# Kernel tuning notes

Measured on AMD Instinct MI355X. Metric: run time of the kernel, lower is better.

The kernel has to match this reference:

```python
import jax, jax.numpy as jnp
import numpy as np

B, C, L = 2, 256, 2048   # batch, emb_dim, seq_len
D, H = 64, 8             # d_model (per-head), n_heads
HD = D * H
EPS = 1e-8


def glob_ln(x, gamma, beta):
    # x: (B, C, L); normalize over all non-batch dims, affine over channel dim 1
    mean = jnp.mean(x, axis=(1, 2), keepdims=True)
    var = jnp.mean((x - mean) ** 2, axis=(1, 2), keepdims=True)
    normed = (x - mean) / jnp.sqrt(var + EPS)
    return gamma[None, :, None] * normed + beta[None, :, None]


def pos_encoding(length, dim):
    pos = jnp.arange(length, dtype=jnp.float32)[:, None]
    div = jnp.exp(jnp.arange(0, dim, 2, dtype=jnp.float32) * (-np.log(10000.0) / dim))
    ang = pos * div  # (L, dim/2)
    return jnp.stack([jnp.sin(ang), jnp.cos(ang)], axis=-1).reshape(length, dim)


def setup_inputs() -> dict:
    key = jax.random.key(0)
    ks = jax.random.split(key, 16)
    s_in = 1.0 / np.sqrt(C)
    s_hd = 1.0 / np.sqrt(HD)
    return {
        "x": jax.random.normal(ks[0], (B, C, L), dtype=jnp.float32),
        "Wq": jax.random.uniform(ks[1], (HD, C), minval=-s_in, maxval=s_in),
        "bq": jax.random.uniform(ks[2], (HD,), minval=-s_in, maxval=s_in),
        "Wk": jax.random.uniform(ks[3], (HD, C), minval=-s_in, maxval=s_in),
        "bk": jax.random.uniform(ks[4], (HD,), minval=-s_in, maxval=s_in),
        "Wv": jax.random.uniform(ks[5], (HD, C), minval=-s_in, maxval=s_in),
        "bv": jax.random.uniform(ks[6], (HD,), minval=-s_in, maxval=s_in),
        "Wo": jax.random.uniform(ks[7], (C, HD), minval=-s_hd, maxval=s_hd),
        "bo": jax.random.uniform(ks[8], (C,), minval=-s_hd, maxval=s_hd),
        "g_mha": jnp.ones((C,)), "b_mha": jnp.zeros((C,)),
        "conv_w": jax.random.uniform(ks[9], (C, C), minval=-s_in, maxval=s_in),
        "conv_b": jax.random.uniform(ks[10], (C,), minval=-s_in, maxval=s_in),
        "g_ffn": jnp.ones((C,)), "b_ffn": jnp.zeros((C,)),
        "alpha": jnp.float32(0.25),
        "g_out": jnp.ones((C,)), "b_out": jnp.zeros((C,)),
    }


def reference(x, Wq, bq, Wk, bk, Wv, bv, Wo, bo, g_mha, b_mha,
              conv_w, conv_b, g_ffn, b_ffn, alpha, g_out, b_out):
    scale = 1.0 / np.sqrt(D)
    t = jnp.transpose(x, (0, 2, 1))            # (B, L, C)
    t = t + pos_encoding(L, C)[None]
    # multi-head attention (self)
    q = (scale * (t @ Wq.T + bq)).reshape(B, L, H, D)
    k = (t @ Wk.T + bk).reshape(B, L, H, D)
    v = (t @ Wv.T + bv).reshape(B, L, H, D)
    scores = jnp.einsum('nlhd,nshd->nhls', q, k)  # (B, H, L, L)
    attn = jax.nn.softmax(scores, axis=-1)
    o = jnp.einsum('nhls,nshd->nlhd', attn, v).reshape(B, L, HD)
    t = t + (o @ Wo.T + bo)                    # residual
    y = glob_ln(jnp.transpose(t, (0, 2, 1)), g_mha, b_mha)  # (B, C, L)
    # FFN: 1x1 conv + GlobLN + PReLU
    f = jnp.einsum('bcl,oc->bol', y, conv_w) + conv_b[None, :, None]
    f = glob_ln(f, g_ffn, b_ffn)
    f = jnp.where(f >= 0, f, alpha * f)
    return glob_ln(f + y, g_out, b_out)
```

## Files before the change

### kernel.cpp

```cpp
#include <hip/hip_runtime.h>
#include <hip/hip_bf16.h>
#include <math.h>

#define BB   2
#define CC   256
#define LL   2048
#define DD   64
#define HH   8
#define HDIM 512
#define BLQ  (BB*LL)
#define EPSV 1e-8f
#define QSCALE (0.125f * 1.44269504088896f)

typedef __attribute__((ext_vector_type(8))) short short8;
typedef __attribute__((ext_vector_type(4))) float f32x4;

__device__ __forceinline__ float wred_sum(float v) {
#pragma unroll
    for (int off = 32; off > 0; off >>= 1) v += __shfl_down(v, off, 64);
    return v;
}
__device__ __forceinline__ unsigned pk(float a, float b) {
    unsigned r;
    asm("v_cvt_pk_bf16_f32 %0, %1, %2" : "=v"(r) : "v"(a), "v"(b));
    return r;
}
__device__ __forceinline__ float ex2(float x) {
    float r;
    asm("v_exp_f32 %0, %1" : "=v"(r) : "v"(x));
    return r;
}
__device__ __forceinline__ float lg2(float x) {
    float r;
    asm("v_log_f32 %0, %1" : "=v"(r) : "v"(x));
    return r;
}
__device__ __forceinline__ float bf2f(unsigned short v) {
    union { unsigned u; float f; } c; c.u = ((unsigned)v) << 16; return c.f;
}
__device__ __forceinline__ short8 ld_frag(const unsigned short* p) {
    union { short8 v; uint2 u[2]; } f;
    f.u[0] = *(const uint2*)p;
    f.u[1] = *(const uint2*)(p + 4);
    return f.v;
}

__global__ __launch_bounds__(256) void k_prep(const float* __restrict__ x,
                                              const float* __restrict__ Wq, const float* __restrict__ Wk,
                                              const float* __restrict__ Wv, const float* __restrict__ Wo,
                                              const float* __restrict__ Wc,
                                              float* __restrict__ t,
                                              unsigned short* __restrict__ tb,
                                              unsigned short* __restrict__ dqkv,
                                              unsigned short* __restrict__ dWo,
                                              unsigned short* __restrict__ dWc) {
    int bid = blockIdx.x;
    int tid = threadIdx.x;
    if (bid >= 256) {
        int idx = ((bid - 256) * 256 + tid) * 4;
        const float* s; unsigned short* d;
        if (idx < 131072)      { s = Wq + idx;          d = dqkv + idx; }
        else if (idx < 262144) { s = Wk + idx - 131072; d = dqkv + idx; }
        else if (idx < 393216) { s = Wv + idx - 262144; d = dqkv + idx; }
        else if (idx < 524288) { s = Wo + idx - 393216; d = dWo + idx - 393216; }
        else                   { s = Wc + idx - 524288; d = dWc + idx - 524288; }
        float4 v = *(const float4*)s;
        uint2 u; u.x = pk(v.x, v.y); u.y = pk(v.z, v.w);
        *(uint2*)d = u;
        return;
    }
    __shared__ float tr[64][65];
    int l0 = (bid & 31) * 64, c0 = ((bid >> 5) & 3) * 64, b = bid >> 7;
    int r = tid >> 2, q = tid & 3;
#pragma unroll
    for (int p = 0; p < 4; ++p) {
        int lc = 4 * (q + 4 * p);
        float4 v = *(const float4*)&x[((size_t)(b * CC + c0 + r)) * LL + l0 + lc];
        tr[lc + 0][r] = v.x; tr[lc + 1][r] = v.y; tr[lc + 2][r] = v.z; tr[lc + 3][r] = v.w;
    }
    __syncthreads();
    int lg = l0 + r;
#pragma unroll
    for (int p = 0; p < 4; ++p) {
        int cc = 4 * (q + 4 * p);
        float4 v = *(const float4*)&tr[r][cc];
        float pe[4];
#pragma unroll
        for (int i = 0; i < 4; ++i) {
            int cg = c0 + cc + i;
            float freq = __expf((float)(cg & ~1) * (-9.210340371976184f / (float)CC));
            float ang = (float)lg * freq;
            pe[i] = (cg & 1) ? __cosf(ang) : __sinf(ang);
        }
        v.x += pe[0]; v.y += pe[1]; v.z += pe[2]; v.w += pe[3];
        size_t o = ((size_t)(b * LL + lg)) * CC + c0 + cc;
        *(float4*)&t[o] = v;
        uint2 u; u.x = pk(v.x, v.y); u.y = pk(v.z, v.w);
        *(uint2*)&tb[o] = u;
    }
}

#define MLDK 68
__global__ __launch_bounds__(256) void k_mm(const unsigned short* __restrict__ A,
                                            const unsigned short* __restrict__ W,
                                            const float* __restrict__ b0,
                                            const float* __restrict__ b1,
                                            const float* __restrict__ b2,
                                            const float* resid,
                                            float* out, unsigned short* outb,
                                            float* pstat,
                                            int mode, int M, int N, int K) {
    __shared__ unsigned short As[2][64][MLDK];
    __shared__ unsigned short Ws[2][64][MLDK];
    __shared__ float rs[4][2];
    int tid = threadIdx.x;
    int w = tid >> 6, lane = tid & 63, g = lane >> 4, qi = lane & 15;
    int bm = blockIdx.x * 64, bn = blockIdx.y * 64;
    int wr = w >> 1, wc = w & 1;
    int srow = tid >> 2, sq = tid & 3;
    bool vseg = (mode == 1) && (bn >= 1024);
    f32x4 acc[2][2];
    acc[0][0] = acc[0][1] = acc[1][0] = acc[1][1] = (f32x4){0.f, 0.f, 0.f, 0.f};
    uint4 ra[2], rw[2];
#pragma unroll
    for (int p = 0; p < 2; ++p) {
        ra[p] = *(const uint4*)&A[(size_t)(bm + srow) * K + (sq + 4 * p) * 8];
        rw[p] = *(const uint4*)&W[(size_t)(bn + srow) * K + (sq + 4 * p) * 8];
    }
    int nt = K >> 6;
    for (int it = 0; it < nt; ++it) {
        int buf = it & 1;
#pragma unroll
        for (int p = 0; p < 2; ++p) {
            *(uint2*)&As[buf][srow][(sq + 4 * p) * 8]     = make_uint2(ra[p].x, ra[p].y);
            *(uint2*)&As[buf][srow][(sq + 4 * p) * 8 + 4] = make_uint2(ra[p].z, ra[p].w);
            *(uint2*)&Ws[buf][srow][(sq + 4 * p) * 8]     = make_uint2(rw[p].x, rw[p].y);
            *(uint2*)&Ws[buf][srow][(sq + 4 * p) * 8 + 4] = make_uint2(rw[p].z, rw[p].w);
        }
        __syncthreads();
        if (it + 1 < nt) {
            int k0 = (it + 1) << 6;
#pragma unroll
            for (int p = 0; p < 2; ++p) {
                ra[p] = *(const uint4*)&A[(size_t)(bm + srow) * K + k0 + (sq + 4 * p) * 8];
                rw[p] = *(const uint4*)&W[(size_t)(bn + srow) * K + k0 + (sq + 4 * p) * 8];
            }
        }
#pragma unroll
        for (int c = 0; c < 2; ++c) {
            short8 wf0 = ld_frag(&Ws[buf][wr * 32 + 0  + qi][c * 32 + 8 * g]);
            short8 wf1 = ld_frag(&Ws[buf][wr * 32 + 16 + qi][c * 32 + 8 * g]);
            short8 af0 = ld_frag(&As[buf][wc * 32 + 0  + qi][c * 32 + 8 * g]);
            short8 af1 = ld_frag(&As[buf][wc * 32 + 16 + qi][c * 32 + 8 * g]);
            if (!vseg) {
                acc[0][0] = __builtin_amdgcn_mfma_f32_16x16x32_bf16(wf0, af0, acc[0][0], 0, 0, 0);
                acc[0][1] = __builtin_amdgcn_mfma_f32_16x16x32_bf16(wf0, af1, acc[0][1], 0, 0, 0);
                acc[1][0] = __builtin_amdgcn_mfma_f32_16x16x32_bf16(wf1, af0, acc[1][0], 0, 0, 0);
                acc[1][1] = __builtin_amdgcn_mfma_f32_16x16x32_bf16(wf1, af1, acc[1][1], 0, 0, 0);
            } else {
                acc[0][0] = __builtin_amdgcn_mfma_f32_16x16x32_bf16(af0, wf0, acc[0][0], 0, 0, 0);
                acc[0][1] = __builtin_amdgcn_mfma_f32_16x16x32_bf16(af0, wf1, acc[0][1], 0, 0, 0);
                acc[1][0] = __builtin_amdgcn_mfma_f32_16x16x32_bf16(af1, wf0, acc[1][0], 0, 0, 0);
                acc[1][1] = __builtin_amdgcn_mfma_f32_16x16x32_bf16(af1, wf1, acc[1][1], 0, 0, 0);
            }
        }
    }
    if (mode == 0) {
        float s = 0.f, s2 = 0.f;
#pragma unroll
        for (int fi = 0; fi < 2; ++fi)
#pragma unroll
            for (int fj = 0; fj < 2; ++fj) {
                int n0 = bn + wr * 32 + fi * 16 + 4 * g;
                int m  = bm + wc * 32 + fj * 16 + qi;
                float4 bi = *(const float4*)&b0[n0];
                float4 v;
                v.x = acc[fi][fj][0] + bi.x; v.y = acc[fi][fj][1] + bi.y;
                v.z = acc[fi][fj][2] + bi.z; v.w = acc[fi][fj][3] + bi.w;
                if (resid) {
                    float4 rv = *(const float4*)&resid[(size_t)m * N + n0];
                    v.x += rv.x; v.y += rv.y; v.z += rv.z; v.w += rv.w;
                }
                *(float4*)&out[(size_t)m * N + n0] = v;
                s  += (v.x + v.y) + (v.z + v.w);
                s2 += v.x * v.x + v.y * v.y + v.z * v.z + v.w * v.w;
            }
        if (pstat) {
            s = wred_sum(s); s2 = wred_sum(s2);
            if (lane == 0) { rs[w][0] = s; rs[w][1] = s2; }
            __syncthreads();
            if (tid == 0) {
                int bid = blockIdx.y * gridDim.x + blockIdx.x;
                pstat[bid * 2 + 0] = rs[0][0] + rs[1][0] + rs[2][0] + rs[3][0];
                pstat[bid * 2 + 1] = rs[0][1] + rs[1][1] + rs[2][1] + rs[3][1];
            }
        }
    } else if (!vseg) {
        int seg = bn >> 9;
        const float* bs = seg ? b1 : b0;
        float sc = seg ? 1.f : QSCALE;
#pragma unroll
        for (int fi = 0; fi < 2; ++fi)
#pragma unroll
            for (int fj = 0; fj < 2; ++fj) {
                int nn0 = (bn & 511) + wr * 32 + fi * 16 + 4 * g;
                int m   = bm + wc * 32 + fj * 16 + qi;
                int b = m >> 11, l = m & (LL - 1);
                int h = nn0 >> 6, d0 = nn0 & 63;
                float4 bi = *(const float4*)&bs[nn0];
                uint2 u;
                u.x = pk(sc * (acc[fi][fj][0] + bi.x), sc * (acc[fi][fj][1] + bi.y));
                u.y = pk(sc * (acc[fi][fj][2] + bi.z), sc * (acc[fi][fj][3] + bi.w));
                *(uint2*)&outb[(size_t)seg * 2097152 +
                               (((size_t)(b * HH + h)) * LL + l) * DD + d0] = u;
            }
    } else {
#pragma unroll
        for (int fi = 0; fi < 2; ++fi)
#pragma unroll
            for (int fj = 0; fj < 2; ++fj) {
                int m0 = bm + wc * 32 + fi * 16 + 4 * g;
                int nn = (bn & 511) + wr * 32 + fj * 16 + qi;
                int b = m0 >> 11, l0 = m0 & (LL - 1);
                int h = nn >> 6, d = nn & 63;
                float bi = b2[nn];
                uint2 u;
                u.x = pk(acc[fi][fj][0] + bi, acc[fi][fj][1] + bi);
                u.y = pk(acc[fi][fj][2] + bi, acc[fi][fj][3] + bi);
                *(uint2*)&outb[(size_t)2 * 2097152 +
                               (((size_t)(b * HH + h)) * DD + d) * LL + l0] = u;
            }
    }
}

#define LDK 68
__global__ __launch_bounds__(256) void k_attn(const unsigned short* __restrict__ QKV,
                                              unsigned short* __restrict__ op0,
                                              unsigned short* __restrict__ op1,
                                              float* __restrict__ ls) {
    int bh = blockIdx.x;
    int h = bh & 7, b = bh >> 3;
    int z = blockIdx.z;
    int sb0 = z << 10;
    int tid = threadIdx.x;
    int w = tid >> 6, lane = tid & 63, g = lane >> 4, qi = lane & 15;
    int q0 = blockIdx.y * 64 + w * 16;
    __shared__ unsigned short Ks[2][64][LDK];
    __shared__ unsigned short Vts[2][64][LDK];
    __shared__ unsigned short Pw[4][16][LDK];
    const unsigned short* Qg = QKV + (size_t)bh * LL * DD;
    const unsigned short* Kg = QKV + 2097152 + (size_t)bh * LL * DD;
    const unsigned short* Vg = QKV + (size_t)2 * 2097152 + (size_t)bh * DD * LL;

    short8 qf[2];
#pragma unroll
    for (int c = 0; c < 2; ++c)
        qf[c] = *(const short8*)&Qg[(size_t)(q0 + qi) * DD + c * 32 + 8 * g];

    f32x4 ot[4];
#pragma unroll
    for (int db = 0; db < 4; ++db) ot[db] = (f32x4){0.f, 0.f, 0.f, 0.f};
    float m = -INFINITY, sum = 0.f;

    int srow = tid >> 2, sq = tid & 3;
    uint4 kr[2], vr[2];
#pragma unroll
    for (int p = 0; p < 2; ++p) {
        kr[p] = *(const uint4*)&Kg[(size_t)(sb0 + srow) * DD + (sq + 4 * p) * 8];
        vr[p] = *(const uint4*)&Vg[(size_t)srow * LL + sb0 + (sq + 4 * p) * 8];
    }
    for (int it = 0; it < 16; ++it) {
        int buf = it & 1;
#pragma unroll
        for (int p = 0; p < 2; ++p) {
            *(uint2*)&Ks[buf][srow][(sq + 4 * p) * 8]      = make_uint2(kr[p].x, kr[p].y);
            *(uint2*)&Ks[buf][srow][(sq + 4 * p) * 8 + 4]  = make_uint2(kr[p].z, kr[p].w);
            *(uint2*)&Vts[buf][srow][(sq + 4 * p) * 8]     = make_uint2(vr[p].x, vr[p].y);
            *(uint2*)&Vts[buf][srow][(sq + 4 * p) * 8 + 4] = make_uint2(vr[p].z, vr[p].w);
        }
        __syncthreads();
        if (it + 1 < 16) {
            int s1 = sb0 + (it + 1) * 64;
#pragma unroll
            for (int p = 0; p < 2; ++p) {
                kr[p] = *(const uint4*)&Kg[(size_t)(s1 + srow) * DD + (sq + 4 * p) * 8];
                vr[p] = *(const uint4*)&Vg[(size_t)srow * LL + s1 + (sq + 4 * p) * 8];
            }
        }
        f32x4 st[4];
        __builtin_amdgcn_s_setprio(1);
#pragma unroll
        for (int sb = 0; sb < 4; ++sb) {
            f32x4 a = (f32x4){0.f, 0.f, 0.f, 0.f};
#pragma unroll
            for (int c = 0; c < 2; ++c) {
                short8 kf = ld_frag(&Ks[buf][sb * 16 + qi][c * 32 + 8 * g]);
                a = __builtin_amdgcn_mfma_f32_16x16x32_bf16(kf, qf[c], a, 0, 0, 0);
            }
            st[sb] = a;
        }
        __builtin_amdgcn_s_setprio(0);
        float t0 = fmaxf(fmaxf(st[0][0], st[0][1]), fmaxf(st[0][2], st[0][3]));
        float t1 = fmaxf(fmaxf(st[1][0], st[1][1]), fmaxf(st[1][2], st[1][3]));
        float t2 = fmaxf(fmaxf(st[2][0], st[2][1]), fmaxf(st[2][2], st[2][3]));
        float t3 = fmaxf(fmaxf(st[3][0], st[3][1]), fmaxf(st[3][2], st[3][3]));
        float tmax = fmaxf(fmaxf(t0, t1), fmaxf(t2, t3));
        tmax = fmaxf(tmax, __shfl_xor(tmax, 16, 64));
        tmax = fmaxf(tmax, __shfl_xor(tmax, 32, 64));
        if (!__all(tmax - m <= 8.f)) {
            float mnew = fmaxf(m, tmax);
            float corr = ex2(m - mnew);
            m = mnew;
            sum *= corr;
#pragma unroll
            for (int db = 0; db < 4; ++db)
#pragma unroll
                for (int r = 0; r < 4; ++r) ot[db][r] *= corr;
        }
        float ps = 0.f;
#pragma unroll
        for (int sb = 0; sb < 4; ++sb) {
            float p0 = ex2(st[sb][0] - m);
            float p1 = ex2(st[sb][1] - m);
            float p2 = ex2(st[sb][2] - m);
            float p3 = ex2(st[sb][3] - m);
            ps += (p0 + p1) + (p2 + p3);
            uint2 w2; w2.x = pk(p0, p1); w2.y = pk(p2, p3);
            *(uint2*)&Pw[w][qi][sb * 16 + 4 * g] = w2;
        }
        sum += ps;
        __builtin_amdgcn_s_setprio(1);
#pragma unroll
        for (int db = 0; db < 4; ++db)
#pragma unroll
            for (int sc = 0; sc < 2; ++sc) {
                short8 vf = ld_frag(&Vts[buf][db * 16 + qi][sc * 32 + 8 * g]);
                short8 pf = ld_frag(&Pw[w][qi][sc * 32 + 8 * g]);
                ot[db] = __builtin_amdgcn_mfma_f32_16x16x32_bf16(vf, pf, ot[db], 0, 0, 0);
            }
        __builtin_amdgcn_s_setprio(0);
    }
    sum += __shfl_xor(sum, 16, 64);
    sum += __shfl_xor(sum, 32, 64);
    float rinv = 1.f / sum;
    unsigned short* op = z ? op1 : op0;
#pragma unroll
    for (int db = 0; db < 4; ++db) {
        int d0 = db * 16 + 4 * g;
        uint2 u;
        u.x = pk(ot[db][0] * rinv, ot[db][1] * rinv);
        u.y = pk(ot[db][2] * rinv, ot[db][3] * rinv);
        *(uint2*)&op[((size_t)(b * LL + q0 + qi)) * HDIM + h * DD + d0] = u;
    }
    if (g == 0) ls[(z << 15) + bh * LL + q0 + qi] = m + lg2(sum);
}

__global__ __launch_bounds__(256) void k_amerge(const unsigned short* op0,
                                                const unsigned short* op1,
                                                const float* __restrict__ ls,
                                                unsigned short* out) {
    int flat = (blockIdx.x * 256 + threadIdx.x) * 8;
    int tt = flat >> 9;
    int h  = (flat >> 6) & 7;
    int b  = tt >> 11, l = tt & (LL - 1);
    int bh = b * HH + h;
    float l0 = ls[bh * LL + l];
    float l1 = ls[(1 << 15) + bh * LL + l];
    float M  = fmaxf(l0, l1);
    float w0 = ex2(l0 - M), w1 = ex2(l1 - M);
    float inv = 1.f / (w0 + w1);
    w0 *= inv; w1 *= inv;
    uint4 a = *(const uint4*)&op0[flat];
    uint4 c = *(const uint4*)&op1[flat];
    const unsigned* au = (const unsigned*)&a;
    const unsigned* cu = (const unsigned*)&c;
    uint4 r;
    unsigned* ru = (unsigned*)&r;
#pragma unroll
    for (int i = 0; i < 4; ++i) {
        float a0 = bf2f((unsigned short)(au[i] & 0xffff));
        float a1 = bf2f((unsigned short)(au[i] >> 16));
        float c0 = bf2f((unsigned short)(cu[i] & 0xffff));
        float c1 = bf2f((unsigned short)(cu[i] >> 16));
        ru[i] = pk(w0 * a0 + w1 * c0, w0 * a1 + w1 * c1);
    }
    *(uint4*)&out[flat] = r;
}

__global__ __launch_bounds__(256) void k_ln(const float* in,
                                            const float* __restrict__ g,
                                            const float* __restrict__ be,
                                            const float* __restrict__ pin,
                                            const float* __restrict__ add,
                                            const float* __restrict__ alpha_ptr,
                                            float* out, unsigned short* outb,
                                            float* pout) {
    __shared__ float rs[4][2];
    int tid = threadIdx.x;
    int b = blockIdx.x >> 9;
    float s = 0.f, s2 = 0.f;
    if (tid < 128) {
        int pidx = (tid >> 5) * 64 + b * 32 + (tid & 31);
        s  = pin[pidx * 2 + 0];
        s2 = pin[pidx * 2 + 1];
    }
    s = wred_sum(s); s2 = wred_sum(s2);
    if ((tid & 63) == 0 && tid < 128) { rs[tid >> 6][0] = s; rs[tid >> 6][1] = s2; }
    __syncthreads();
    float S = rs[0][0] + rs[1][0], S2 = rs[0][1] + rs[1][1];
    float mean = S / (float)(CC * LL);
    float inv  = rsqrtf(S2 / (float)(CC * LL) - mean * mean + EPSV);

    int idx = (blockIdx.x * 256 + tid) * 4;
    int c = idx & (CC - 1);
    float4 v  = *(const float4*)&in[idx];
    float4 gg = *(const float4*)&g[c];
    float4 bb = *(const float4*)&be[c];
    v.x = (v.x - mean) * inv * gg.x + bb.x;
    v.y = (v.y - mean) * inv * gg.y + bb.y;
    v.z = (v.z - mean) * inv * gg.z + bb.z;
    v.w = (v.w - mean) * inv * gg.w + bb.w;
    if (alpha_ptr) {
        float al = alpha_ptr[0];
        v.x = v.x >= 0.f ? v.x : al * v.x;
        v.y = v.y >= 0.f ? v.y : al * v.y;
        v.z = v.z >= 0.f ? v.z : al * v.z;
        v.w = v.w >= 0.f ? v.w : al * v.w;
    }
    if (add) {
        float4 a = *(const float4*)&add[idx];
        v.x += a.x; v.y += a.y; v.z += a.z; v.w += a.w;
    }
    *(float4*)&out[idx] = v;
    if (outb) {
        uint2 u; u.x = pk(v.x, v.y); u.y = pk(v.z, v.w);
        *(uint2*)&outb[idx] = u;
    }
    if (pout) {
        float os  = (v.x + v.y) + (v.z + v.w);
        float os2 = v.x * v.x + v.y * v.y + v.z * v.z + v.w * v.w;
        os = wred_sum(os); os2 = wred_sum(os2);
        __syncthreads();
        if ((tid & 63) == 0) { rs[tid >> 6][0] = os; rs[tid >> 6][1] = os2; }
        __syncthreads();
        if (tid == 0) {
            pout[blockIdx.x * 2 + 0] = rs[0][0] + rs[1][0] + rs[2][0] + rs[3][0];
            pout[blockIdx.x * 2 + 1] = rs[0][1] + rs[1][1] + rs[2][1] + rs[3][1];
        }
    }
}

__global__ __launch_bounds__(256) void k_ln_t(const float* __restrict__ in,
                                              const float* __restrict__ g,
                                              const float* __restrict__ be,
                                              const float* __restrict__ pin,
                                              float* __restrict__ out) {
    __shared__ float tr[64][65];
    __shared__ float rs[4][2];
    int l0 = blockIdx.x * 64, c0 = blockIdx.y * 64, b = blockIdx.z;
    int tid = threadIdx.x, r = tid >> 2, q = tid & 3;
    float s  = pin[(b * 512 + tid) * 2 + 0] + pin[(b * 512 + 256 + tid) * 2 + 0];
    float s2 = pin[(b * 512 + tid) * 2 + 1] + pin[(b * 512 + 256 + tid) * 2 + 1];
    s = wred_sum(s); s2 = wred_sum(s2);
    if ((tid & 63) == 0) { rs[tid >> 6][0] = s; rs[tid >> 6][1] = s2; }
    __syncthreads();
    float S = rs[0][0] + rs[1][0] + rs[2][0] + rs[3][0];
    float S2 = rs[0][1] + rs[1][1] + rs[2][1] + rs[3][1];
    float mean = S / (float)(CC * LL);
    float inv  = rsqrtf(S2 / (float)(CC * LL) - mean * mean + EPSV);
#pragma unroll
    for (int p = 0; p < 4; ++p) {
        int cc = 4 * (q + 4 * p);
        float4 v  = *(const float4*)&in[((size_t)(b * LL + l0 + r)) * CC + c0 + cc];
        float4 gg = *(const float4*)&g[c0 + cc];
        float4 bb = *(const float4*)&be[c0 + cc];
        tr[cc + 0][r] = (v.x - mean) * inv * gg.x + bb.x;
        tr[cc + 1][r] = (v.y - mean) * inv * gg.y + bb.y;
        tr[cc + 2][r] = (v.z - mean) * inv * gg.z + bb.z;
        tr[cc + 3][r] = (v.w - mean) * inv * gg.w + bb.w;
    }
    __syncthreads();
#pragma unroll
    for (int p = 0; p < 4; ++p) {
        int ll = 4 * (q + 4 * p);
        float4 v = *(const float4*)&tr[r][ll];
        *(float4*)&out[((size_t)(b * CC + c0 + r)) * LL + l0 + ll] = v;
    }
}

extern "C" void kernel_launch(void* const* d_in, const int* in_sizes, int n_in,
                              void* d_out, int out_size, void* d_ws, size_t ws_size,
                              hipStream_t stream) {
    const float* x      = (const float*)d_in[0];
    const float* Wq     = (const float*)d_in[1];
    const float* bq     = (const float*)d_in[2];
    const float* Wk     = (const float*)d_in[3];
    const float* bk     = (const float*)d_in[4];
    const float* Wv     = (const float*)d_in[5];
    const float* bv     = (const float*)d_in[6];
    const float* Wo     = (const float*)d_in[7];
    const float* bo     = (const float*)d_in[8];
    const float* g_mha  = (const float*)d_in[9];
    const float* b_mha  = (const float*)d_in[10];
    const float* conv_w = (const float*)d_in[11];
    const float* conv_b = (const float*)d_in[12];
    const float* g_ffn  = (const float*)d_in[13];
    const float* b_ffn  = (const float*)d_in[14];
    const float* alpha  = (const float*)d_in[15];
    const float* g_out  = (const float*)d_in[16];
    const float* b_out  = (const float*)d_in[17];
    float* out = (float*)d_out;

    float* ws = (float*)d_ws;
    float* t             = ws;
    unsigned short* tb   = (unsigned short*)(ws + 1048576);
    unsigned short* QKVb = (unsigned short*)(ws + 1572864);
    float* f             = ws + 1572864;
    unsigned short* ybf  = (unsigned short*)(ws + 2621440);
    unsigned short* obuf = (unsigned short*)(ws + 4718592);
    unsigned short* Wqkvb= (unsigned short*)(ws + 5767168);
    unsigned short* Wob  = (unsigned short*)(ws + 5963776);
    unsigned short* Wcb  = (unsigned short*)(ws + 6029312);
    float* pstatA        = ws + 6062080;
    float* pstatB        = ws + 6062592;
    float* pstatC        = ws + 6063104;
    unsigned short* op1  = (unsigned short*)(ws + 6065152);
    float* lsbuf         = ws + 7113728;

    k_prep<<<832, 256, 0, stream>>>(x, Wq, Wk, Wv, Wo, conv_w, t, tb, Wqkvb, Wob, Wcb);

    dim3 gqkv(BLQ / 64, 1536 / 64);
    k_mm<<<gqkv, 256, 0, stream>>>(tb, Wqkvb, bq, bk, bv, nullptr, nullptr, QKVb,
                                   nullptr, 1, BLQ, 1536, CC);

    dim3 gattn(HH * BB, LL / 64, 2);
    k_attn<<<gattn, 256, 0, stream>>>(QKVb, obuf, op1, lsbuf);
    k_amerge<<<1024, 256, 0, stream>>>(obuf, op1, lsbuf, obuf);

    dim3 go(BLQ / 64, CC / 64);
    k_mm<<<go, 256, 0, stream>>>(obuf, Wob, bo, nullptr, nullptr, t, t, nullptr,
                                 pstatA, 0, BLQ, CC, HDIM);

    k_ln<<<1024, 256, 0, stream>>>(t, g_mha, b_mha, pstatA, nullptr, nullptr,
                                   t, ybf, nullptr);

    k_mm<<<go, 256, 0, stream>>>(ybf, Wcb, conv_b, nullptr, nullptr, nullptr, f, nullptr,
                                 pstatB, 0, BLQ, CC, CC);

    k_ln<<<1024, 256, 0, stream>>>(f, g_ffn, b_ffn, pstatB, t, alpha,
                                   f, nullptr, pstatC);

    k_ln_t<<<dim3(LL / 64, CC / 64, BB), 256, 0, stream>>>(f, g_out, b_out, pstatC, out);
}
```

Baseline: 94.64 us.

## Switch attention to 32x32x16 MFMA with register-resident P via permlane swap

The attention kernel now uses 32x32x16 bf16 MFMA tiles, so each wave handles 32 queries and each block 128. The softmax probabilities are repacked in registers with v_permlane32_swap instead of a round trip through the shared-memory Pw buffer. Each K/V tile loaded into LDS is therefore reused by twice as many queries, and the LDS traffic and syncs for P go away. In exchange the grid is halved (fewer blocks, lower occupancy) and register pressure grows with two 16-wide accumulators.

```diff
diff --git a/kernel.cpp b/kernel.cpp
--- a/kernel.cpp
+++ b/kernel.cpp
@@ -14,6 +14,7 @@
 
 typedef __attribute__((ext_vector_type(8))) short short8;
 typedef __attribute__((ext_vector_type(4))) float f32x4;
+typedef __attribute__((ext_vector_type(16))) float f32x16;
 
 __device__ __forceinline__ float wred_sum(float v) {
 #pragma unroll
@@ -37,6 +38,14 @@
 }
 __device__ __forceinline__ float bf2f(unsigned short v) {
     union { unsigned u; float f; } c; c.u = ((unsigned)v) << 16; return c.f;
+}
+__device__ __forceinline__ void pswap(unsigned &x, unsigned &y) {
+    asm("v_permlane32_swap_b32 %0, %1" : "+v"(x), "+v"(y));
+}
+__device__ __forceinline__ short8 mk8(unsigned x0, unsigned x1, unsigned x2, unsigned x3) {
+    union { short8 v; unsigned u[4]; } r;
+    r.u[0] = x0; r.u[1] = x1; r.u[2] = x2; r.u[3] = x3;
+    return r.v;
 }
 __device__ __forceinline__ short8 ld_frag(const unsigned short* p) {
     union { short8 v; uint2 u[2]; } f;
@@ -243,23 +252,23 @@
     int z = blockIdx.z;
     int sb0 = z << 10;
     int tid = threadIdx.x;
-    int w = tid >> 6, lane = tid & 63, g = lane >> 4, qi = lane & 15;
-    int q0 = blockIdx.y * 64 + w * 16;
+    int w = tid >> 6, lane = tid & 63;
+    int lo31 = lane & 31, hi = lane >> 5;
+    int q0 = blockIdx.y * 128 + w * 32;
     __shared__ unsigned short Ks[2][64][LDK];
     __shared__ unsigned short Vts[2][64][LDK];
-    __shared__ unsigned short Pw[4][16][LDK];
     const unsigned short* Qg = QKV + (size_t)bh * LL * DD;
     const unsigned short* Kg = QKV + 2097152 + (size_t)bh * LL * DD;
     const unsigned short* Vg = QKV + (size_t)2 * 2097152 + (size_t)bh * DD * LL;
 
-    short8 qf[2];
-#pragma unroll
-    for (int c = 0; c < 2; ++c)
-        qf[c] = *(const short8*)&Qg[(size_t)(q0 + qi) * DD + c * 32 + 8 * g];
-
-    f32x4 ot[4];
-#pragma unroll
-    for (int db = 0; db < 4; ++db) ot[db] = (f32x4){0.f, 0.f, 0.f, 0.f};
+    short8 qf[4];
+#pragma unroll
+    for (int c = 0; c < 4; ++c)
+        qf[c] = *(const short8*)&Qg[(size_t)(q0 + lo31) * DD + c * 16 + 8 * hi];
+
+    f32x16 o0, o1;
+#pragma unroll
+    for (int r = 0; r < 16; ++r) { o0[r] = 0.f; o1[r] = 0.f; }
     float m = -INFINITY, sum = 0.f;
 
     int srow = tid >> 2, sq = tid & 3;
@@ -287,72 +296,74 @@
                 vr[p] = *(const uint4*)&Vg[(size_t)srow * LL + s1 + (sq + 4 * p) * 8];
             }
         }
-        f32x4 st[4];
-        __builtin_amdgcn_s_setprio(1);
-#pragma unroll
-        for (int sb = 0; sb < 4; ++sb) {
-            f32x4 a = (f32x4){0.f, 0.f, 0.f, 0.f};
-#pragma unroll
-            for (int c = 0; c < 2; ++c) {
-                short8 kf = ld_frag(&Ks[buf][sb * 16 + qi][c * 32 + 8 * g]);
-                a = __builtin_amdgcn_mfma_f32_16x16x32_bf16(kf, qf[c], a, 0, 0, 0);
-            }
-            st[sb] = a;
-        }
-        __builtin_amdgcn_s_setprio(0);
-        float t0 = fmaxf(fmaxf(st[0][0], st[0][1]), fmaxf(st[0][2], st[0][3]));
-        float t1 = fmaxf(fmaxf(st[1][0], st[1][1]), fmaxf(st[1][2], st[1][3]));
-        float t2 = fmaxf(fmaxf(st[2][0], st[2][1]), fmaxf(st[2][2], st[2][3]));
-        float t3 = fmaxf(fmaxf(st[3][0], st[3][1]), fmaxf(st[3][2], st[3][3]));
-        float tmax = fmaxf(fmaxf(t0, t1), fmaxf(t2, t3));
-        tmax = fmaxf(tmax, __shfl_xor(tmax, 16, 64));
-        tmax = fmaxf(tmax, __shfl_xor(tmax, 32, 64));
-        if (!__all(tmax - m <= 8.f)) {
-            float mnew = fmaxf(m, tmax);
-            float corr = ex2(m - mnew);
-            m = mnew;
-            sum *= corr;
-#pragma unroll
-            for (int db = 0; db < 4; ++db)
-#pragma unroll
-                for (int r = 0; r < 4; ++r) ot[db][r] *= corr;
-        }
-        float ps = 0.f;
-#pragma unroll
-        for (int sb = 0; sb < 4; ++sb) {
-            float p0 = ex2(st[sb][0] - m);
-            float p1 = ex2(st[sb][1] - m);
-            float p2 = ex2(st[sb][2] - m);
-            float p3 = ex2(st[sb][3] - m);
-            ps += (p0 + p1) + (p2 + p3);
-            uint2 w2; w2.x = pk(p0, p1); w2.y = pk(p2, p3);
-            *(uint2*)&Pw[w][qi][sb * 16 + 4 * g] = w2;
-        }
-        sum += ps;
-        __builtin_amdgcn_s_setprio(1);
-#pragma unroll
-        for (int db = 0; db < 4; ++db)
-#pragma unroll
-            for (int sc = 0; sc < 2; ++sc) {
-                short8 vf = ld_frag(&Vts[buf][db * 16 + qi][sc * 32 + 8 * g]);
-                short8 pf = ld_frag(&Pw[w][qi][sc * 32 + 8 * g]);
-                ot[db] = __builtin_amdgcn_mfma_f32_16x16x32_bf16(vf, pf, ot[db], 0, 0, 0);
-            }
-        __builtin_amdgcn_s_setprio(0);
-    }
-    sum += __shfl_xor(sum, 16, 64);
+#pragma unroll
+        for (int sub = 0; sub < 2; ++sub) {
+            f32x16 st;
+#pragma unroll
+            for (int r = 0; r < 16; ++r) st[r] = 0.f;
+            __builtin_amdgcn_s_setprio(1);
+#pragma unroll
+            for (int c = 0; c < 4; ++c) {
+                short8 kf = ld_frag(&Ks[buf][sub * 32 + lo31][c * 16 + 8 * hi]);
+                st = __builtin_amdgcn_mfma_f32_32x32x16_bf16(kf, qf[c], st, 0, 0, 0);
+            }
+            __builtin_amdgcn_s_setprio(0);
+            float t0 = fmaxf(fmaxf(st[0], st[1]),   fmaxf(st[2], st[3]));
+            float t1 = fmaxf(fmaxf(st[4], st[5]),   fmaxf(st[6], st[7]));
+            float t2 = fmaxf(fmaxf(st[8], st[9]),   fmaxf(st[10], st[11]));
+            float t3 = fmaxf(fmaxf(st[12], st[13]), fmaxf(st[14], st[15]));
+            float tmax = fmaxf(fmaxf(t0, t1), fmaxf(t2, t3));
+            tmax = fmaxf(tmax, __shfl_xor(tmax, 32, 64));
+            if (!__all(tmax - m <= 8.f)) {
+                float mnew = fmaxf(m, tmax);
+                float corr = ex2(m - mnew);
+                m = mnew;
+                sum *= corr;
+#pragma unroll
+                for (int r = 0; r < 16; ++r) { o0[r] *= corr; o1[r] *= corr; }
+            }
+            float p[16];
+#pragma unroll
+            for (int r = 0; r < 16; ++r) { p[r] = ex2(st[r] - m); sum += p[r]; }
+            unsigned pa = pk(p[0], p[1]),   pb = pk(p[2], p[3]);
+            unsigned pc = pk(p[4], p[5]),   pd = pk(p[6], p[7]);
+            pswap(pc, pa); pswap(pd, pb);
+            unsigned pe = pk(p[8], p[9]),   pf = pk(p[10], p[11]);
+            unsigned pg = pk(p[12], p[13]), ph = pk(p[14], p[15]);
+            pswap(pg, pe); pswap(ph, pf);
+            short8 pb0 = mk8(pa, pb, pc, pd);
+            short8 pb1 = mk8(pe, pf, pg, ph);
+            __builtin_amdgcn_s_setprio(1);
+            {
+                short8 vf00 = ld_frag(&Vts[buf][lo31][sub * 32 + 8 * hi]);
+                short8 vf01 = ld_frag(&Vts[buf][lo31][sub * 32 + 16 + 8 * hi]);
+                short8 vf10 = ld_frag(&Vts[buf][32 + lo31][sub * 32 + 8 * hi]);
+                short8 vf11 = ld_frag(&Vts[buf][32 + lo31][sub * 32 + 16 + 8 * hi]);
+                o0 = __builtin_amdgcn_mfma_f32_32x32x16_bf16(vf00, pb0, o0, 0, 0, 0);
+                o0 = __builtin_amdgcn_mfma_f32_32x32x16_bf16(vf01, pb1, o0, 0, 0, 0);
+                o1 = __builtin_amdgcn_mfma_f32_32x32x16_bf16(vf10, pb0, o1, 0, 0, 0);
+                o1 = __builtin_amdgcn_mfma_f32_32x32x16_bf16(vf11, pb1, o1, 0, 0, 0);
+            }
+            __builtin_amdgcn_s_setprio(0);
+        }
+    }
     sum += __shfl_xor(sum, 32, 64);
     float rinv = 1.f / sum;
     unsigned short* op = z ? op1 : op0;
-#pragma unroll
-    for (int db = 0; db < 4; ++db) {
-        int d0 = db * 16 + 4 * g;
+    size_t base = ((size_t)(b * LL + q0 + lo31)) * HDIM + h * DD;
+#pragma unroll
+    for (int j = 0; j < 4; ++j) {
+        int d0 = 8 * j + 4 * hi;
         uint2 u;
-        u.x = pk(ot[db][0] * rinv, ot[db][1] * rinv);
-        u.y = pk(ot[db][2] * rinv, ot[db][3] * rinv);
-        *(uint2*)&op[((size_t)(b * LL + q0 + qi)) * HDIM + h * DD + d0] = u;
-    }
-    if (g == 0) ls[(z << 15) + bh * LL + q0 + qi] = m + lg2(sum);
+        u.x = pk(o0[4 * j + 0] * rinv, o0[4 * j + 1] * rinv);
+        u.y = pk(o0[4 * j + 2] * rinv, o0[4 * j + 3] * rinv);
+        *(uint2*)&op[base + d0] = u;
+        uint2 u1;
+        u1.x = pk(o1[4 * j + 0] * rinv, o1[4 * j + 1] * rinv);
+        u1.y = pk(o1[4 * j + 2] * rinv, o1[4 * j + 3] * rinv);
+        *(uint2*)&op[base + 32 + d0] = u1;
+    }
+    if (hi == 0) ls[(z << 15) + bh * LL + q0 + lo31] = m + lg2(sum);
 }
 
 __global__ __launch_bounds__(256) void k_amerge(const unsigned short* op0,
@@ -533,7 +544,7 @@
     k_mm<<<gqkv, 256, 0, stream>>>(tb, Wqkvb, bq, bk, bv, nullptr, nullptr, QKVb,
                                    nullptr, 1, BLQ, 1536, CC);
 
-    dim3 gattn(HH * BB, LL / 64, 2);
+    dim3 gattn(HH * BB, LL / 128, 2);
     k_attn<<<gattn, 256, 0, stream>>>(QKVb, obuf, op1, lsbuf);
     k_amerge<<<1024, 256, 0, stream>>>(obuf, op1, lsbuf, obuf);
 
```

Measured after the change: 82.90 us. 12.4% less time.
